# Kernel optimization log

Hardware: AMD Instinct MI355X
Metric: run time of the kernel (lower is better)

## Reference

```python
import jax, jax.numpy as jnp
import numpy as np

B, T, HID = 2, 4096, 1024
NH, DK, DV = 8, 128, 128
CONV_K = 4
CHUNK = 64


def short_conv_silu(x, w):
    # causal depthwise conv1d, x: [B,T,D], w: [D,K]
    K = w.shape[1]
    xp = jnp.pad(x, ((0, 0), (K - 1, 0), (0, 0)))
    out = sum(xp[:, i:i + x.shape[1], :] * w[:, i] for i in range(K))
    return jax.nn.silu(out)


def hadamard_fm(x, w1, b1, w2, b2):
    # per-head feature map: Linear(x)*Linear(x), x: [B,T,H,D]
    return (jnp.einsum('bthd,ed->bthe', x, w1) + b1) * (jnp.einsum('bthd,ed->bthe', x, w2) + b2)


def chunk_linear_attn(q, k, v, scale):
    # causal linear attention via chunked scan. q,k,v: [B,T,H,D]
    Bq, Tq, H, Dk = q.shape
    Dv = v.shape[-1]
    nc = Tq // CHUNK
    q = (q * scale).reshape(Bq, nc, CHUNK, H, Dk).transpose(1, 0, 2, 3, 4)
    k = k.reshape(Bq, nc, CHUNK, H, Dk).transpose(1, 0, 2, 3, 4)
    v = v.reshape(Bq, nc, CHUNK, H, Dv).transpose(1, 0, 2, 3, 4)
    mask = jnp.tril(jnp.ones((CHUNK, CHUNK), dtype=bool))

    def step(S, inp):
        qc, kc, vc = inp  # [B,C,H,D]
        attn = jnp.einsum('bihk,bjhk->bhij', qc, kc)
        attn = jnp.where(mask, attn, 0.0)
        o = jnp.einsum('bhij,bjhv->bihv', attn, vc) + jnp.einsum('bihk,bhkv->bihv', qc, S)
        S = S + jnp.einsum('bihk,bihv->bhkv', kc, vc)
        return S, o

    S0 = jnp.zeros((Bq, H, Dk, Dv), q.dtype)
    _, o = jax.lax.scan(step, S0, (q, k, v))  # o: [nc,B,C,H,Dv]
    return o.transpose(1, 0, 2, 3, 4).reshape(Bq, Tq, H, Dv)


def setup_inputs() -> dict:
    key = jax.random.key(0)
    ks = jax.random.split(key, 16)
    s = 0.02
    inp = {
        'hidden_states': jax.random.normal(ks[0], (B, T, HID), jnp.float32),
        'wq': jax.random.normal(ks[1], (HID, HID), jnp.float32) * s,
        'wk': jax.random.normal(ks[2], (HID, HID), jnp.float32) * s,
        'wv': jax.random.normal(ks[3], (HID, HID), jnp.float32) * s,
        'wo': jax.random.normal(ks[4], (HID, HID), jnp.float32) * s,
        'conv_q': jax.random.normal(ks[5], (HID, CONV_K), jnp.float32) * 0.2,
        'conv_k': jax.random.normal(ks[6], (HID, CONV_K), jnp.float32) * 0.2,
        'conv_v': jax.random.normal(ks[7], (HID, CONV_K), jnp.float32) * 0.2,
        'fmq_w1': jax.random.normal(ks[8], (DK, DK), jnp.float32) * s,
        'fmq_b1': jnp.zeros((DK,), jnp.float32),
        'fmq_w2': jax.random.normal(ks[9], (DK, DK), jnp.float32) * s,
        'fmq_b2': jnp.zeros((DK,), jnp.float32),
        'fmk_w1': jax.random.normal(ks[10], (DK, DK), jnp.float32) * s,
        'fmk_b1': jnp.zeros((DK,), jnp.float32),
        'fmk_w2': jax.random.normal(ks[11], (DK, DK), jnp.float32) * s,
        'fmk_b2': jnp.zeros((DK,), jnp.float32),
    }
    return inp


def reference(hidden_states, wq, wk, wv, wo, conv_q, conv_k, conv_v,
              fmq_w1, fmq_b1, fmq_w2, fmq_b2, fmk_w1, fmk_b1, fmk_w2, fmk_b2):
    q = short_conv_silu(hidden_states @ wq.T, conv_q)
    k = short_conv_silu(hidden_states @ wk.T, conv_k)
    v = short_conv_silu(hidden_states @ wv.T, conv_v)
    q = q.reshape(B, T, NH, DK)
    k = k.reshape(B, T, NH, DK)
    v = v.reshape(B, T, NH, DV)
    q = hadamard_fm(q, fmq_w1, fmq_b1, fmq_w2, fmq_b2)
    k = hadamard_fm(k, fmk_w1, fmk_b1, fmk_w2, fmk_b2)
    scale = DK ** -0.5
    o = chunk_linear_attn(q, k, v, scale)
    return o.reshape(B, T, NH * DV) @ wo.T
```

## Files before the change

kernel.cpp:

```cpp
#include <hip/hip_runtime.h>
#include <cstdint>
#include <cstddef>

#define T_SEQ 4096
#define BATCH 2
#define HIDDEN 1024
#define NHEAD 8
#define DKV 128
#define BT (BATCH * T_SEQ)
#define NCH 64
#define CHUNK_L 64
#define QSCALE 0.08838834764831845f
#define SCALE_P 1024.0f
#define SCALE_O 8192.0f
#define OEPS 0.7071067811865476f

typedef _Float16 half8 __attribute__((ext_vector_type(8)));
typedef float floatx4 __attribute__((ext_vector_type(4)));

union HBits { _Float16 h; unsigned short u; };

__global__ void cast_f32_f16(const float* __restrict__ X, _Float16* __restrict__ Y, int n8)
{
    int idx = blockIdx.x * 256 + threadIdx.x;
    if (idx < n8) {
        float4 a = ((const float4*)X)[idx * 2];
        float4 b = ((const float4*)X)[idx * 2 + 1];
        half8 h = { (_Float16)a.x, (_Float16)a.y, (_Float16)a.z, (_Float16)a.w,
                    (_Float16)b.x, (_Float16)b.y, (_Float16)b.z, (_Float16)b.w };
        *(half8*)&Y[idx * 8] = h;
    }
}

__global__ void cast4_f32_f16(const float* __restrict__ A, const float* __restrict__ B,
                              const float* __restrict__ C, const float* __restrict__ D,
                              _Float16* __restrict__ a, _Float16* __restrict__ b,
                              _Float16* __restrict__ c, _Float16* __restrict__ d, int n8)
{
    int sel = blockIdx.y;
    const float* src = (sel == 0) ? A : (sel == 1) ? B : (sel == 2) ? C : D;
    _Float16* dst = (sel == 0) ? a : (sel == 1) ? b : (sel == 2) ? c : d;
    int idx = blockIdx.x * 256 + threadIdx.x;
    if (idx < n8) {
        float4 u = ((const float4*)src)[idx * 2];
        float4 v = ((const float4*)src)[idx * 2 + 1];
        half8 h = { (_Float16)u.x, (_Float16)u.y, (_Float16)u.z, (_Float16)u.w,
                    (_Float16)v.x, (_Float16)v.y, (_Float16)v.z, (_Float16)v.w };
        *(half8*)&dst[idx * 8] = h;
    }
}

__global__ __launch_bounds__(256) void gemm_nt_f16_h16(const _Float16* __restrict__ A,
                                                       const _Float16* __restrict__ W,
                                                       _Float16* __restrict__ C,
                                                       int M, int N, int K)
{
    __shared__ _Float16 As[128 * 64];
    __shared__ _Float16 Ws[128 * 64];
    const int bm = blockIdx.y * 128;
    const int bn = blockIdx.x * 128;
    const int tid = threadIdx.x;
    const int w = tid >> 6;
    const int l = tid & 63;
    const int wm = (w >> 1) * 64;
    const int wn = (w & 1) * 64;
    const int lane16 = l & 15;
    const int quad = l >> 4;
    const int srow = w * 8 + (l >> 3);
    const int skh = ((l & 7) ^ (l >> 3)) * 8;
    const int rsw = lane16 & 7;

    floatx4 acc[4][4];
#pragma unroll
    for (int i = 0; i < 4; ++i)
#pragma unroll
        for (int j = 0; j < 4; ++j)
            acc[i][j] = (floatx4){0.f, 0.f, 0.f, 0.f};

    for (int k0 = 0; k0 < K; k0 += 64) {
#pragma unroll
        for (int c = 0; c < 4; ++c) {
            int row = c * 32 + srow;
            const _Float16* ga = A + (size_t)(bm + row) * K + k0 + skh;
            const _Float16* gw = W + (size_t)(bn + row) * K + k0 + skh;
            __builtin_amdgcn_global_load_lds(
                (const __attribute__((address_space(1))) void*)ga,
                (__attribute__((address_space(3))) void*)(As + c * 2048 + w * 512), 16, 0, 0);
            __builtin_amdgcn_global_load_lds(
                (const __attribute__((address_space(1))) void*)gw,
                (__attribute__((address_space(3))) void*)(Ws + c * 2048 + w * 512), 16, 0, 0);
        }
        __syncthreads();

#pragma unroll
        for (int s = 0; s < 2; ++s) {
            const int pc = (((s * 4 + quad) ^ rsw)) * 8;
            half8 a[4], b[4];
#pragma unroll
            for (int i = 0; i < 4; ++i) {
                a[i] = *(const half8*)&As[(wm + i * 16 + lane16) * 64 + pc];
                b[i] = *(const half8*)&Ws[(wn + i * 16 + lane16) * 64 + pc];
            }
#pragma unroll
            for (int i = 0; i < 4; ++i)
#pragma unroll
                for (int j = 0; j < 4; ++j)
                    acc[i][j] = __builtin_amdgcn_mfma_f32_16x16x32_f16(a[i], b[j], acc[i][j], 0, 0, 0);
        }
        __syncthreads();
    }
#pragma unroll
    for (int i = 0; i < 4; ++i)
#pragma unroll
        for (int j = 0; j < 4; ++j)
#pragma unroll
            for (int r = 0; r < 4; ++r)
                C[(size_t)(bm + wm + i * 16 + quad * 4 + r) * N + bn + wn + j * 16 + lane16] =
                    (_Float16)acc[i][j][r];
}

__global__ __launch_bounds__(256) void gemm_nt_f16_f32(const _Float16* __restrict__ A,
                                                       const _Float16* __restrict__ W,
                                                       float* __restrict__ C,
                                                       int M, int N, int K, float scale)
{
    __shared__ _Float16 As[128 * 64];
    __shared__ _Float16 Ws[128 * 64];
    const int bm = blockIdx.y * 128;
    const int bn = blockIdx.x * 128;
    const int tid = threadIdx.x;
    const int w = tid >> 6;
    const int l = tid & 63;
    const int wm = (w >> 1) * 64;
    const int wn = (w & 1) * 64;
    const int lane16 = l & 15;
    const int quad = l >> 4;
    const int srow = w * 8 + (l >> 3);
    const int skh = ((l & 7) ^ (l >> 3)) * 8;
    const int rsw = lane16 & 7;

    floatx4 acc[4][4];
#pragma unroll
    for (int i = 0; i < 4; ++i)
#pragma unroll
        for (int j = 0; j < 4; ++j)
            acc[i][j] = (floatx4){0.f, 0.f, 0.f, 0.f};

    for (int k0 = 0; k0 < K; k0 += 64) {
#pragma unroll
        for (int c = 0; c < 4; ++c) {
            int row = c * 32 + srow;
            const _Float16* ga = A + (size_t)(bm + row) * K + k0 + skh;
            const _Float16* gw = W + (size_t)(bn + row) * K + k0 + skh;
            __builtin_amdgcn_global_load_lds(
                (const __attribute__((address_space(1))) void*)ga,
                (__attribute__((address_space(3))) void*)(As + c * 2048 + w * 512), 16, 0, 0);
            __builtin_amdgcn_global_load_lds(
                (const __attribute__((address_space(1))) void*)gw,
                (__attribute__((address_space(3))) void*)(Ws + c * 2048 + w * 512), 16, 0, 0);
        }
        __syncthreads();

#pragma unroll
        for (int s = 0; s < 2; ++s) {
            const int pc = (((s * 4 + quad) ^ rsw)) * 8;
            half8 a[4], b[4];
#pragma unroll
            for (int i = 0; i < 4; ++i) {
                a[i] = *(const half8*)&As[(wm + i * 16 + lane16) * 64 + pc];
                b[i] = *(const half8*)&Ws[(wn + i * 16 + lane16) * 64 + pc];
            }
#pragma unroll
            for (int i = 0; i < 4; ++i)
#pragma unroll
                for (int j = 0; j < 4; ++j)
                    acc[i][j] = __builtin_amdgcn_mfma_f32_16x16x32_f16(a[i], b[j], acc[i][j], 0, 0, 0);
        }
        __syncthreads();
    }
#pragma unroll
    for (int i = 0; i < 4; ++i)
#pragma unroll
        for (int j = 0; j < 4; ++j)
#pragma unroll
            for (int r = 0; r < 4; ++r)
                C[(size_t)(bm + wm + i * 16 + quad * 4 + r) * N + bn + wn + j * 16 + lane16] =
                    acc[i][j][r] * scale;
}

#define CSTRIPE 16
__global__ __launch_bounds__(256) void conv_silu_col2(const _Float16* __restrict__ X, int ldx,
                                                      const float* __restrict__ Wq,
                                                      const float* __restrict__ Wk,
                                                      _Float16* __restrict__ Yq,
                                                      _Float16* __restrict__ Yk)
{
    const int sel = blockIdx.y;
    const _Float16* Xs = X + sel * HIDDEN;
    const float* Wc = sel ? Wk : Wq;
    _Float16* Y = sel ? Yk : Yq;

    int gid = blockIdx.x * 256 + threadIdx.x;
    int c = gid & 127;
    int sg = gid >> 7;
    int r0 = sg * CSTRIPE;
    int tloc = r0 & (T_SEQ - 1);
    int d0 = c * 8;

    float w0[8], w1[8], w2[8], w3[8];
#pragma unroll
    for (int e = 0; e < 8; ++e) {
        float4 wv = *(const float4*)&Wc[(d0 + e) * 4];
        w0[e] = wv.x; w1[e] = wv.y; w2[e] = wv.z; w3[e] = wv.w;
    }

    half8 xm1 = {0,0,0,0,0,0,0,0}, xm2 = xm1, xm3 = xm1;
    if (tloc >= 1) xm1 = *(const half8*)&Xs[(size_t)(r0 - 1) * ldx + d0];
    if (tloc >= 2) xm2 = *(const half8*)&Xs[(size_t)(r0 - 2) * ldx + d0];
    if (tloc >= 3) xm3 = *(const half8*)&Xs[(size_t)(r0 - 3) * ldx + d0];

    for (int i = 0; i < CSTRIPE; ++i) {
        half8 x0 = *(const half8*)&Xs[(size_t)(r0 + i) * ldx + d0];
        half8 o;
#pragma unroll
        for (int e = 0; e < 8; ++e) {
            float acc = fmaf((float)x0[e], w3[e],
                        fmaf((float)xm1[e], w2[e],
                        fmaf((float)xm2[e], w1[e], (float)xm3[e] * w0[e])));
            o[e] = (_Float16)(acc / (1.f + __expf(-acc)));
        }
        *(half8*)&Y[(size_t)(r0 + i) * HIDDEN + d0] = o;
        xm3 = xm2; xm2 = xm1; xm1 = x0;
    }
}

__global__ __launch_bounds__(256) void conv_silu_T(const _Float16* __restrict__ X, int ldx,
                                                   const float* __restrict__ Wc,
                                                   _Float16* __restrict__ VT)
{
    __shared__ _Float16 xs[67 * 64];
    const int t0 = blockIdx.x * 64;
    const int dt = blockIdx.y * 64;
    const int z = blockIdx.z;
    const int tid = threadIdx.x;

#pragma unroll
    for (int i = 0; i < 3; ++i) {
        int p = tid + 256 * i;
        if (p < 536) {
            int row = p >> 3, d8 = (p & 7) * 8;
            int t = t0 - 3 + row;
            half8 v;
            if (t >= 0)
                v = *(const half8*)&X[((size_t)z * T_SEQ + t) * ldx + dt + d8];
            else
                v = (half8){0, 0, 0, 0, 0, 0, 0, 0};
            *(half8*)&xs[row * 64 + d8] = v;
        }
    }
    __syncthreads();

    const int d = tid & 63;
    const int dg = dt + d;
    float4 w = *(const float4*)&Wc[dg * 4];
#pragma unroll
    for (int u = 0; u < 2; ++u) {
        int tg = (tid >> 6) + u * 4;
        half8 o;
#pragma unroll
        for (int s = 0; s < 8; ++s) {
            int base = (tg * 8 + s + 3) * 64 + d;
            float acc = (float)xs[base] * w.w
                      + (float)xs[base - 64] * w.z
                      + (float)xs[base - 128] * w.y
                      + (float)xs[base - 192] * w.x;
            o[s] = (_Float16)(acc / (1.f + __expf(-acc)));
        }
        *(half8*)&VT[((size_t)z * HIDDEN + dg) * T_SEQ + t0 + tg * 8] = o;
    }
}

__global__ __launch_bounds__(256) void fm_mfma2(const _Float16* __restrict__ Xq,
                                                const _Float16* __restrict__ Xk,
                                                const _Float16* __restrict__ Wfm,
                                                const float* __restrict__ Bq1,
                                                const float* __restrict__ Bq2,
                                                const float* __restrict__ Bk1,
                                                const float* __restrict__ Bk2,
                                                _Float16* __restrict__ OUTq,
                                                _Float16* __restrict__ OUTk)
{
    const int sel = blockIdx.z;
    const _Float16* X = sel ? Xk : Xq;
    const _Float16* W1h = Wfm + (sel ? 2 * 16384 : 0);
    const _Float16* W2h = Wfm + (sel ? 3 * 16384 : 16384);
    const float* B1 = sel ? Bk1 : Bq1;
    const float* B2 = sel ? Bk2 : Bq2;
    _Float16* OUT = sel ? OUTk : OUTq;

    __shared__ _Float16 xs[4 * 64 * 32];
    const int t0 = blockIdx.x * 64;
    const int h = blockIdx.y;
    const int tid = threadIdx.x;
    const int w = tid >> 6;
    const int l = tid & 63;
    const int lane16 = l & 15;
    const int quad = l >> 4;

#pragma unroll
    for (int c = 0; c < 4; ++c) {
        int row = c * 16 + (l >> 2);
        const _Float16* g = X + (size_t)(t0 + row) * HIDDEN + h * DKV + w * 32 + (l & 3) * 8;
        __builtin_amdgcn_global_load_lds(
            (const __attribute__((address_space(1))) void*)g,
            (__attribute__((address_space(3))) void*)(xs + w * 2048 + c * 512), 16, 0, 0);
    }
    __syncthreads();

    floatx4 acc1[4][2], acc2[4][2];
#pragma unroll
    for (int i = 0; i < 4; ++i)
#pragma unroll
        for (int j = 0; j < 2; ++j) {
            acc1[i][j] = (floatx4){0.f, 0.f, 0.f, 0.f};
            acc2[i][j] = (floatx4){0.f, 0.f, 0.f, 0.f};
        }

#pragma unroll
    for (int s = 0; s < 4; ++s) {
        half8 a[4];
#pragma unroll
        for (int mt = 0; mt < 4; ++mt)
            a[mt] = *(const half8*)&xs[s * 2048 + (mt * 16 + lane16) * 32 + quad * 8];
#pragma unroll
        for (int nt = 0; nt < 2; ++nt) {
            int e = w * 32 + nt * 16 + lane16;
            half8 b1 = *(const half8*)&W1h[(size_t)e * DKV + s * 32 + quad * 8];
            half8 b2 = *(const half8*)&W2h[(size_t)e * DKV + s * 32 + quad * 8];
#pragma unroll
            for (int mt = 0; mt < 4; ++mt) {
                acc1[mt][nt] = __builtin_amdgcn_mfma_f32_16x16x32_f16(a[mt], b1, acc1[mt][nt], 0, 0, 0);
                acc2[mt][nt] = __builtin_amdgcn_mfma_f32_16x16x32_f16(a[mt], b2, acc2[mt][nt], 0, 0, 0);
            }
        }
    }

#pragma unroll
    for (int nt = 0; nt < 2; ++nt) {
        int e = w * 32 + nt * 16 + lane16;
        float b1v = B1[e], b2v = B2[e];
#pragma unroll
        for (int mt = 0; mt < 4; ++mt)
#pragma unroll
            for (int r = 0; r < 4; ++r) {
                float o = (acc1[mt][nt][r] + b1v) * (acc2[mt][nt][r] + b2v);
                OUT[(size_t)(t0 + mt * 16 + quad * 4 + r) * HIDDEN + h * DKV + e] = (_Float16)o;
            }
    }
}

__global__ __launch_bounds__(256) void ktv_mfma(const _Float16* __restrict__ Kf,
                                                const _Float16* __restrict__ VT,
                                                float* __restrict__ G)
{
    __shared__ _Float16 kt[128 * 72];
    const int c = blockIdx.x;
    const int bh = blockIdx.y;
    const int b = bh >> 3, h = bh & 7;
    const int tid = threadIdx.x;
    const int w = tid >> 6;
    const int l = tid & 63;
    const int lane16 = l & 15;
    const int quad = l >> 4;
    const size_t rowbase = (size_t)b * T_SEQ + (size_t)c * CHUNK_L;

    {
        const int dk0 = (tid >> 4) * 8;
        const int jb = (tid & 15) * 4;
        half8 r0 = *(const half8*)&Kf[(rowbase + jb + 0) * HIDDEN + h * DKV + dk0];
        half8 r1 = *(const half8*)&Kf[(rowbase + jb + 1) * HIDDEN + h * DKV + dk0];
        half8 r2 = *(const half8*)&Kf[(rowbase + jb + 2) * HIDDEN + h * DKV + dk0];
        half8 r3 = *(const half8*)&Kf[(rowbase + jb + 3) * HIDDEN + h * DKV + dk0];
#pragma unroll
        for (int dk = 0; dk < 8; ++dk) {
            HBits a0, a1, a2, a3;
            a0.h = r0[dk]; a1.h = r1[dk]; a2.h = r2[dk]; a3.h = r3[dk];
            unsigned int lo = ((unsigned int)a1.u << 16) | a0.u;
            unsigned int hi = ((unsigned int)a3.u << 16) | a2.u;
            *(unsigned int*)&kt[(dk0 + dk) * 72 + jb] = lo;
            *(unsigned int*)&kt[(dk0 + dk) * 72 + jb + 2] = hi;
        }
    }
    __syncthreads();

    const int m0 = (w >> 1) * 64;
    const int n0 = (w & 1) * 64;
    floatx4 acc[4][4];
#pragma unroll
    for (int i = 0; i < 4; ++i)
#pragma unroll
        for (int j = 0; j < 4; ++j)
            acc[i][j] = (floatx4){0.f, 0.f, 0.f, 0.f};

#pragma unroll
    for (int s = 0; s < 2; ++s) {
        half8 a[4], bb[4];
#pragma unroll
        for (int mt = 0; mt < 4; ++mt) {
            int dv = m0 + mt * 16 + lane16;
            a[mt] = *(const half8*)&VT[((size_t)bh * DKV + dv) * T_SEQ + c * CHUNK_L + s * 32 + quad * 8];
        }
#pragma unroll
        for (int nt = 0; nt < 4; ++nt)
            bb[nt] = *(const half8*)&kt[(n0 + nt * 16 + lane16) * 72 + s * 32 + quad * 8];
#pragma unroll
        for (int mt = 0; mt < 4; ++mt)
#pragma unroll
            for (int nt = 0; nt < 4; ++nt)
                acc[mt][nt] = __builtin_amdgcn_mfma_f32_16x16x32_f16(a[mt], bb[nt], acc[mt][nt], 0, 0, 0);
    }

    float* Gp = G + ((size_t)bh * NCH + c) * (DKV * DKV);
#pragma unroll
    for (int mt = 0; mt < 4; ++mt)
#pragma unroll
        for (int nt = 0; nt < 4; ++nt)
#pragma unroll
            for (int r = 0; r < 4; ++r)
                Gp[(size_t)(m0 + mt * 16 + quad * 4 + r) * DKV + n0 + nt * 16 + lane16] =
                    acc[mt][nt][r];
}

__global__ void prefix_kernel(const float* __restrict__ G, _Float16* __restrict__ Gh)
{
    int idx = blockIdx.x * 256 + threadIdx.x;
    int bh = idx >> 14;
    int e = idx & 16383;
    const float* p = G + (size_t)bh * NCH * 16384 + e;
    _Float16* q = Gh + (size_t)bh * NCH * 16384 + e;
    float run = 0.f;
#pragma unroll
    for (int c = 0; c < NCH; ++c) {
        q[(size_t)c * 16384] = (_Float16)(run * SCALE_P);
        run += p[(size_t)c * 16384];
    }
}

#define PSLD 40
__global__ __launch_bounds__(256) void attn_mfma(const _Float16* __restrict__ Qf,
                                                 const _Float16* __restrict__ Kf,
                                                 const _Float16* __restrict__ VT,
                                                 const _Float16* __restrict__ Gh,
                                                 _Float16* __restrict__ O)
{
    __shared__ _Float16 ps[2 * 64 * PSLD];
    const int c = blockIdx.x;
    const int bh = blockIdx.y;
    const int b = bh >> 3, h = bh & 7;
    const int tid = threadIdx.x;
    const int w = tid >> 6;
    const int l = tid & 63;
    const int lane16 = l & 15;
    const int quad = l >> 4;
    const size_t rowbase = (size_t)b * T_SEQ + (size_t)c * CHUNK_L;

    {
        const int m0 = (w >> 1) * 32;
        const int n0 = (w & 1) * 32;
        floatx4 aq[2][2];
#pragma unroll
        for (int i = 0; i < 2; ++i)
#pragma unroll
            for (int j = 0; j < 2; ++j)
                aq[i][j] = (floatx4){0.f, 0.f, 0.f, 0.f};
#pragma unroll
        for (int s = 0; s < 4; ++s) {
            half8 a[2], bb[2];
#pragma unroll
            for (int mt = 0; mt < 2; ++mt)
                a[mt] = *(const half8*)&Qf[(rowbase + m0 + mt * 16 + lane16) * HIDDEN +
                                           h * DKV + s * 32 + quad * 8];
#pragma unroll
            for (int nt = 0; nt < 2; ++nt)
                bb[nt] = *(const half8*)&Kf[(rowbase + n0 + nt * 16 + lane16) * HIDDEN +
                                            h * DKV + s * 32 + quad * 8];
#pragma unroll
            for (int mt = 0; mt < 2; ++mt)
#pragma unroll
                for (int nt = 0; nt < 2; ++nt)
                    aq[mt][nt] = __builtin_amdgcn_mfma_f32_16x16x32_f16(a[mt], bb[nt], aq[mt][nt], 0, 0, 0);
        }
#pragma unroll
        for (int mt = 0; mt < 2; ++mt)
#pragma unroll
            for (int nt = 0; nt < 2; ++nt) {
                int j = n0 + nt * 16 + lane16;
#pragma unroll
                for (int r = 0; r < 4; ++r) {
                    int i = m0 + mt * 16 + quad * 4 + r;
                    float v = (j <= i) ? aq[mt][nt][r] * SCALE_P : 0.f;
                    ps[(j >> 5) * 64 * PSLD + i * PSLD + (j & 31)] = (_Float16)v;
                }
            }
    }
    __syncthreads();

    const int n0o = w * 32;
    floatx4 accO[4][2];
#pragma unroll
    for (int i = 0; i < 4; ++i)
#pragma unroll
        for (int j = 0; j < 2; ++j)
            accO[i][j] = (floatx4){0.f, 0.f, 0.f, 0.f};

#pragma unroll
    for (int s = 0; s < 2; ++s) {
        half8 a[4], bb[2];
#pragma unroll
        for (int mt = 0; mt < 4; ++mt)
            a[mt] = *(const half8*)&ps[s * 64 * PSLD + (mt * 16 + lane16) * PSLD + quad * 8];
#pragma unroll
        for (int nt = 0; nt < 2; ++nt) {
            int dv = n0o + nt * 16 + lane16;
            bb[nt] = *(const half8*)&VT[((size_t)bh * DKV + dv) * T_SEQ + c * CHUNK_L + s * 32 + quad * 8];
        }
#pragma unroll
        for (int mt = 0; mt < 4; ++mt)
#pragma unroll
            for (int nt = 0; nt < 2; ++nt)
                accO[mt][nt] = __builtin_amdgcn_mfma_f32_16x16x32_f16(a[mt], bb[nt], accO[mt][nt], 0, 0, 0);
    }

    const _Float16* gh = Gh + ((size_t)bh * NCH + c) * (DKV * DKV);
#pragma unroll
    for (int s = 0; s < 4; ++s) {
        half8 a[4], bb[2];
#pragma unroll
        for (int mt = 0; mt < 4; ++mt)
            a[mt] = *(const half8*)&Qf[(rowbase + mt * 16 + lane16) * HIDDEN +
                                       h * DKV + s * 32 + quad * 8];
#pragma unroll
        for (int nt = 0; nt < 2; ++nt) {
            int dv = n0o + nt * 16 + lane16;
            bb[nt] = *(const half8*)&gh[(size_t)dv * DKV + s * 32 + quad * 8];
        }
#pragma unroll
        for (int mt = 0; mt < 4; ++mt)
#pragma unroll
            for (int nt = 0; nt < 2; ++nt)
                accO[mt][nt] = __builtin_amdgcn_mfma_f32_16x16x32_f16(a[mt], bb[nt], accO[mt][nt], 0, 0, 0);
    }

#pragma unroll
    for (int mt = 0; mt < 4; ++mt)
#pragma unroll
        for (int nt = 0; nt < 2; ++nt)
#pragma unroll
            for (int r = 0; r < 4; ++r)
                O[(rowbase + mt * 16 + quad * 4 + r) * HIDDEN + h * DKV + n0o + nt * 16 + lane16] =
                    (_Float16)(accO[mt][nt][r] * OEPS);
}

extern "C" void kernel_launch(void* const* d_in, const int* in_sizes, int n_in,
                              void* d_out, int out_size, void* d_ws, size_t ws_size,
                              hipStream_t stream)
{
    (void)in_sizes; (void)n_in; (void)out_size; (void)ws_size;
    const float* hs = (const float*)d_in[0];
    const float* wq = (const float*)d_in[1];
    const float* wk = (const float*)d_in[2];
    const float* wv = (const float*)d_in[3];
    const float* wo = (const float*)d_in[4];
    const float* cq = (const float*)d_in[5];
    const float* ck = (const float*)d_in[6];
    const float* cv = (const float*)d_in[7];
    const float* fmq_w1 = (const float*)d_in[8];
    const float* fmq_b1 = (const float*)d_in[9];
    const float* fmq_w2 = (const float*)d_in[10];
    const float* fmq_b2 = (const float*)d_in[11];
    const float* fmk_w1 = (const float*)d_in[12];
    const float* fmk_b1 = (const float*)d_in[13];
    const float* fmk_w2 = (const float*)d_in[14];
    const float* fmk_b2 = (const float*)d_in[15];
    float* out = (float*)d_out;
    char* ws = (char*)d_ws;

    const size_t MB = 1024 * 1024;
    _Float16* h16     = (_Float16*)(ws + 0);
    _Float16* wqkv16  = (_Float16*)(ws + 16 * MB);
    _Float16* wo16    = wqkv16 + (3 << 20);
    _Float16* fmw     = wqkv16 + (4 << 20);
    _Float16* qkvlin  = (_Float16*)(ws + 32 * MB);
    _Float16* qf16    = (_Float16*)(ws + 32 * MB);
    _Float16* kf16    = (_Float16*)(ws + 48 * MB);
    _Float16* Gh      = (_Float16*)(ws + 64 * MB);
    _Float16* qc16    = (_Float16*)(ws + 80 * MB);
    _Float16* kc16    = (_Float16*)(ws + 96 * MB);
    _Float16* O16     = (_Float16*)(ws + 96 * MB);
    _Float16* vT      = (_Float16*)(ws + 112 * MB);
    float*    G       = (float*)(ws + 128 * MB);

    cast_f32_f16<<<4096, 256, 0, stream>>>(hs, h16, BT * HIDDEN / 8);
    cast4_f32_f16<<<dim3(512, 4), 256, 0, stream>>>(wq, wk, wv, wo,
                                                    wqkv16, wqkv16 + (1 << 20), wqkv16 + (2 << 20), wo16,
                                                    HIDDEN * HIDDEN / 8);
    cast4_f32_f16<<<dim3(8, 4), 256, 0, stream>>>(fmq_w1, fmq_w2, fmk_w1, fmk_w2,
                                                  fmw, fmw + 16384, fmw + 2 * 16384, fmw + 3 * 16384,
                                                  DKV * DKV / 8);

    dim3 gqkv(3 * HIDDEN / 128, BT / 128);
    gemm_nt_f16_h16<<<gqkv, 256, 0, stream>>>(h16, wqkv16, qkvlin, BT, 3 * HIDDEN, HIDDEN);

    conv_silu_col2<<<dim3((128 * (BT / CSTRIPE)) / 256, 2), 256, 0, stream>>>(
        qkvlin, 3 * HIDDEN, cq, ck, qc16, kc16);
    dim3 cg(T_SEQ / 64, HIDDEN / 64, BATCH);
    conv_silu_T<<<cg, 256, 0, stream>>>(qkvlin + 2 * HIDDEN, 3 * HIDDEN, cv, vT);

    dim3 fg(BT / 64, NHEAD, 2);
    fm_mfma2<<<fg, 256, 0, stream>>>(qc16, kc16, fmw, fmq_b1, fmq_b2, fmk_b1, fmk_b2, qf16, kf16);

    dim3 ag(NCH, BATCH * NHEAD);
    ktv_mfma<<<ag, 256, 0, stream>>>(kf16, vT, G);
    prefix_kernel<<<(16 * 16384) / 256, 256, 0, stream>>>(G, Gh);
    attn_mfma<<<ag, 256, 0, stream>>>(qf16, kf16, vT, Gh, O16);

    dim3 gg(HIDDEN / 128, BT / 128);
    gemm_nt_f16_f32<<<gg, 256, 0, stream>>>(O16, wo16, out, BT, HIDDEN, HIDDEN, 1.0f / SCALE_O);
}
```

Baseline: 335.2 us.

## Merge cast and conv launches, store chunk KV states in fp16

The weight-cast launches are combined into one eight-way cast kernel, and the q/k conv and the transposed v conv are merged into a single launch that branches on blockIdx.y. The per-chunk K^T V states are written as fp16 instead of fp32, which halves the traffic between ktv_mfma and the prefix kernel. qf16 is moved to a different workspace offset. The aim is fewer launches and less memory traffic, at the cost of precision in the chunk-state accumulation and some idle blocks in the merged conv grid.

```diff
diff --git a/kernel.cpp b/kernel.cpp
--- a/kernel.cpp
+++ b/kernel.cpp
@@ -32,14 +32,28 @@
     }
 }
 
-__global__ void cast4_f32_f16(const float* __restrict__ A, const float* __restrict__ B,
-                              const float* __restrict__ C, const float* __restrict__ D,
-                              _Float16* __restrict__ a, _Float16* __restrict__ b,
-                              _Float16* __restrict__ c, _Float16* __restrict__ d, int n8)
+__global__ void cast8_f32_f16(const float* __restrict__ s0, const float* __restrict__ s1,
+                              const float* __restrict__ s2, const float* __restrict__ s3,
+                              const float* __restrict__ s4, const float* __restrict__ s5,
+                              const float* __restrict__ s6, const float* __restrict__ s7,
+                              _Float16* __restrict__ d0, _Float16* __restrict__ d1,
+                              _Float16* __restrict__ d2, _Float16* __restrict__ d3,
+                              _Float16* __restrict__ d4, _Float16* __restrict__ d5,
+                              _Float16* __restrict__ d6, _Float16* __restrict__ d7,
+                              int nbig, int nsmall)
 {
     int sel = blockIdx.y;
-    const float* src = (sel == 0) ? A : (sel == 1) ? B : (sel == 2) ? C : D;
-    _Float16* dst = (sel == 0) ? a : (sel == 1) ? b : (sel == 2) ? c : d;
+    const float* src; _Float16* dst; int n8;
+    switch (sel) {
+        case 0: src = s0; dst = d0; n8 = nbig; break;
+        case 1: src = s1; dst = d1; n8 = nbig; break;
+        case 2: src = s2; dst = d2; n8 = nbig; break;
+        case 3: src = s3; dst = d3; n8 = nbig; break;
+        case 4: src = s4; dst = d4; n8 = nsmall; break;
+        case 5: src = s5; dst = d5; n8 = nsmall; break;
+        case 6: src = s6; dst = d6; n8 = nsmall; break;
+        default: src = s7; dst = d7; n8 = nsmall; break;
+    }
     int idx = blockIdx.x * 256 + threadIdx.x;
     if (idx < n8) {
         float4 u = ((const float4*)src)[idx * 2];
@@ -189,60 +203,65 @@
 }
 
 #define CSTRIPE 16
-__global__ __launch_bounds__(256) void conv_silu_col2(const _Float16* __restrict__ X, int ldx,
-                                                      const float* __restrict__ Wq,
-                                                      const float* __restrict__ Wk,
-                                                      _Float16* __restrict__ Yq,
-                                                      _Float16* __restrict__ Yk)
-{
-    const int sel = blockIdx.y;
-    const _Float16* Xs = X + sel * HIDDEN;
-    const float* Wc = sel ? Wk : Wq;
-    _Float16* Y = sel ? Yk : Yq;
-
-    int gid = blockIdx.x * 256 + threadIdx.x;
-    int c = gid & 127;
-    int sg = gid >> 7;
-    int r0 = sg * CSTRIPE;
-    int tloc = r0 & (T_SEQ - 1);
-    int d0 = c * 8;
-
-    float w0[8], w1[8], w2[8], w3[8];
-#pragma unroll
-    for (int e = 0; e < 8; ++e) {
-        float4 wv = *(const float4*)&Wc[(d0 + e) * 4];
-        w0[e] = wv.x; w1[e] = wv.y; w2[e] = wv.z; w3[e] = wv.w;
-    }
-
-    half8 xm1 = {0,0,0,0,0,0,0,0}, xm2 = xm1, xm3 = xm1;
-    if (tloc >= 1) xm1 = *(const half8*)&Xs[(size_t)(r0 - 1) * ldx + d0];
-    if (tloc >= 2) xm2 = *(const half8*)&Xs[(size_t)(r0 - 2) * ldx + d0];
-    if (tloc >= 3) xm3 = *(const half8*)&Xs[(size_t)(r0 - 3) * ldx + d0];
-
-    for (int i = 0; i < CSTRIPE; ++i) {
-        half8 x0 = *(const half8*)&Xs[(size_t)(r0 + i) * ldx + d0];
-        half8 o;
+__global__ __launch_bounds__(256) void conv_silu_all(const _Float16* __restrict__ X, int ldx,
+                                                     const float* __restrict__ Wq,
+                                                     const float* __restrict__ Wk,
+                                                     const float* __restrict__ Wv,
+                                                     _Float16* __restrict__ Yq,
+                                                     _Float16* __restrict__ Yk,
+                                                     _Float16* __restrict__ VT)
+{
+    const int path = blockIdx.y;
+    const int tid = threadIdx.x;
+
+    if (path < 2) {
+        int gid = blockIdx.x * 256 + tid;
+        if (gid >= 128 * (BT / CSTRIPE)) return;
+
+        const _Float16* Xs = X + path * HIDDEN;
+        const float* Wc = path ? Wk : Wq;
+        _Float16* Y = path ? Yk : Yq;
+
+        int c = gid & 127;
+        int sg = gid >> 7;
+        int r0 = sg * CSTRIPE;
+        int tloc = r0 & (T_SEQ - 1);
+        int d0 = c * 8;
+
+        float w0[8], w1[8], w2[8], w3[8];
 #pragma unroll
         for (int e = 0; e < 8; ++e) {
-            float acc = fmaf((float)x0[e], w3[e],
-                        fmaf((float)xm1[e], w2[e],
-                        fmaf((float)xm2[e], w1[e], (float)xm3[e] * w0[e])));
-            o[e] = (_Float16)(acc / (1.f + __expf(-acc)));
-        }
-        *(half8*)&Y[(size_t)(r0 + i) * HIDDEN + d0] = o;
-        xm3 = xm2; xm2 = xm1; xm1 = x0;
-    }
-}
-
-__global__ __launch_bounds__(256) void conv_silu_T(const _Float16* __restrict__ X, int ldx,
-                                                   const float* __restrict__ Wc,
-                                                   _Float16* __restrict__ VT)
-{
+            float4 wv = *(const float4*)&Wc[(d0 + e) * 4];
+            w0[e] = wv.x; w1[e] = wv.y; w2[e] = wv.z; w3[e] = wv.w;
+        }
+
+        half8 xm1 = {0,0,0,0,0,0,0,0}, xm2 = xm1, xm3 = xm1;
+        if (tloc >= 1) xm1 = *(const half8*)&Xs[(size_t)(r0 - 1) * ldx + d0];
+        if (tloc >= 2) xm2 = *(const half8*)&Xs[(size_t)(r0 - 2) * ldx + d0];
+        if (tloc >= 3) xm3 = *(const half8*)&Xs[(size_t)(r0 - 3) * ldx + d0];
+
+        for (int i = 0; i < CSTRIPE; ++i) {
+            half8 x0 = *(const half8*)&Xs[(size_t)(r0 + i) * ldx + d0];
+            half8 o;
+#pragma unroll
+            for (int e = 0; e < 8; ++e) {
+                float acc = fmaf((float)x0[e], w3[e],
+                            fmaf((float)xm1[e], w2[e],
+                            fmaf((float)xm2[e], w1[e], (float)xm3[e] * w0[e])));
+                o[e] = (_Float16)(acc / (1.f + __expf(-acc)));
+            }
+            *(half8*)&Y[(size_t)(r0 + i) * HIDDEN + d0] = o;
+            xm3 = xm2; xm2 = xm1; xm1 = x0;
+        }
+        return;
+    }
+
     __shared__ _Float16 xs[67 * 64];
-    const int t0 = blockIdx.x * 64;
-    const int dt = blockIdx.y * 64;
-    const int z = blockIdx.z;
-    const int tid = threadIdx.x;
+    const int bx = blockIdx.x;
+    const int t0 = (bx & 63) * 64;
+    const int dt = ((bx >> 6) & 15) * 64;
+    const int z = bx >> 10;
+    const _Float16* Xv = X + 2 * HIDDEN;
 
 #pragma unroll
     for (int i = 0; i < 3; ++i) {
@@ -252,7 +271,7 @@
             int t = t0 - 3 + row;
             half8 v;
             if (t >= 0)
-                v = *(const half8*)&X[((size_t)z * T_SEQ + t) * ldx + dt + d8];
+                v = *(const half8*)&Xv[((size_t)z * T_SEQ + t) * ldx + dt + d8];
             else
                 v = (half8){0, 0, 0, 0, 0, 0, 0, 0};
             *(half8*)&xs[row * 64 + d8] = v;
@@ -262,7 +281,7 @@
 
     const int d = tid & 63;
     const int dg = dt + d;
-    float4 w = *(const float4*)&Wc[dg * 4];
+    float4 w = *(const float4*)&Wv[dg * 4];
 #pragma unroll
     for (int u = 0; u < 2; ++u) {
         int tg = (tid >> 6) + u * 4;
@@ -361,7 +380,7 @@
 
 __global__ __launch_bounds__(256) void ktv_mfma(const _Float16* __restrict__ Kf,
                                                 const _Float16* __restrict__ VT,
-                                                float* __restrict__ G)
+                                                _Float16* __restrict__ G16)
 {
     __shared__ _Float16 kt[128 * 72];
     const int c = blockIdx.x;
@@ -420,7 +439,7 @@
                 acc[mt][nt] = __builtin_amdgcn_mfma_f32_16x16x32_f16(a[mt], bb[nt], acc[mt][nt], 0, 0, 0);
     }
 
-    float* Gp = G + ((size_t)bh * NCH + c) * (DKV * DKV);
+    _Float16* Gp = G16 + ((size_t)bh * NCH + c) * (DKV * DKV);
 #pragma unroll
     for (int mt = 0; mt < 4; ++mt)
 #pragma unroll
@@ -428,21 +447,21 @@
 #pragma unroll
             for (int r = 0; r < 4; ++r)
                 Gp[(size_t)(m0 + mt * 16 + quad * 4 + r) * DKV + n0 + nt * 16 + lane16] =
-                    acc[mt][nt][r];
-}
-
-__global__ void prefix_kernel(const float* __restrict__ G, _Float16* __restrict__ Gh)
+                    (_Float16)acc[mt][nt][r];
+}
+
+__global__ void prefix_kernel(const _Float16* __restrict__ G16, _Float16* __restrict__ Gh)
 {
     int idx = blockIdx.x * 256 + threadIdx.x;
     int bh = idx >> 14;
     int e = idx & 16383;
-    const float* p = G + (size_t)bh * NCH * 16384 + e;
+    const _Float16* p = G16 + (size_t)bh * NCH * 16384 + e;
     _Float16* q = Gh + (size_t)bh * NCH * 16384 + e;
     float run = 0.f;
 #pragma unroll
     for (int c = 0; c < NCH; ++c) {
         q[(size_t)c * 16384] = (_Float16)(run * SCALE_P);
-        run += p[(size_t)c * 16384];
+        run += (float)p[(size_t)c * 16384];
     }
 }
 
@@ -591,37 +610,34 @@
     _Float16* wo16    = wqkv16 + (3 << 20);
     _Float16* fmw     = wqkv16 + (4 << 20);
     _Float16* qkvlin  = (_Float16*)(ws + 32 * MB);
-    _Float16* qf16    = (_Float16*)(ws + 32 * MB);
+    _Float16* qf16    = (_Float16*)(ws + 0);
     _Float16* kf16    = (_Float16*)(ws + 48 * MB);
     _Float16* Gh      = (_Float16*)(ws + 64 * MB);
     _Float16* qc16    = (_Float16*)(ws + 80 * MB);
     _Float16* kc16    = (_Float16*)(ws + 96 * MB);
     _Float16* O16     = (_Float16*)(ws + 96 * MB);
     _Float16* vT      = (_Float16*)(ws + 112 * MB);
-    float*    G       = (float*)(ws + 128 * MB);
+    _Float16* G16     = (_Float16*)(ws + 128 * MB);
 
     cast_f32_f16<<<4096, 256, 0, stream>>>(hs, h16, BT * HIDDEN / 8);
-    cast4_f32_f16<<<dim3(512, 4), 256, 0, stream>>>(wq, wk, wv, wo,
-                                                    wqkv16, wqkv16 + (1 << 20), wqkv16 + (2 << 20), wo16,
-                                                    HIDDEN * HIDDEN / 8);
-    cast4_f32_f16<<<dim3(8, 4), 256, 0, stream>>>(fmq_w1, fmq_w2, fmk_w1, fmk_w2,
-                                                  fmw, fmw + 16384, fmw + 2 * 16384, fmw + 3 * 16384,
-                                                  DKV * DKV / 8);
+    cast8_f32_f16<<<dim3(512, 8), 256, 0, stream>>>(
+        wq, wk, wv, wo, fmq_w1, fmq_w2, fmk_w1, fmk_w2,
+        wqkv16, wqkv16 + (1 << 20), wqkv16 + (2 << 20), wo16,
+        fmw, fmw + 16384, fmw + 2 * 16384, fmw + 3 * 16384,
+        HIDDEN * HIDDEN / 8, DKV * DKV / 8);
 
     dim3 gqkv(3 * HIDDEN / 128, BT / 128);
     gemm_nt_f16_h16<<<gqkv, 256, 0, stream>>>(h16, wqkv16, qkvlin, BT, 3 * HIDDEN, HIDDEN);
 
-    conv_silu_col2<<<dim3((128 * (BT / CSTRIPE)) / 256, 2), 256, 0, stream>>>(
-        qkvlin, 3 * HIDDEN, cq, ck, qc16, kc16);
-    dim3 cg(T_SEQ / 64, HIDDEN / 64, BATCH);
-    conv_silu_T<<<cg, 256, 0, stream>>>(qkvlin + 2 * HIDDEN, 3 * HIDDEN, cv, vT);
+    conv_silu_all<<<dim3(2048, 3), 256, 0, stream>>>(
+        qkvlin, 3 * HIDDEN, cq, ck, cv, qc16, kc16, vT);
 
     dim3 fg(BT / 64, NHEAD, 2);
     fm_mfma2<<<fg, 256, 0, stream>>>(qc16, kc16, fmw, fmq_b1, fmq_b2, fmk_b1, fmk_b2, qf16, kf16);
 
     dim3 ag(NCH, BATCH * NHEAD);
-    ktv_mfma<<<ag, 256, 0, stream>>>(kf16, vT, G);
-    prefix_kernel<<<(16 * 16384) / 256, 256, 0, stream>>>(G, Gh);
+    ktv_mfma<<<ag, 256, 0, stream>>>(kf16, vT, G16);
+    prefix_kernel<<<(16 * 16384) / 256, 256, 0, stream>>>(G16, Gh);
     attn_mfma<<<ag, 256, 0, stream>>>(qf16, kf16, vT, Gh, O16);
 
     dim3 gg(HIDDEN / 128, BT / 128);
```

Result: faster. 327.1 us (-2.4%).
